# Optimization experiments

Hardware: AMD Instinct MI355X
Metric: run time of the kernel (lower is better)

Reference implementation:

```python
import jax, jax.numpy as jnp
import numpy as np

N = 20000
NEG_SLOPE = 0.2


def gatv2_layer(x, src, dst, edge_attr, Wl, bl, Wr, br, We, att, bias, H, C):
    """PyG GATv2Conv: add self-loops (edge_attr fill='mean'), gather-score-softmax-aggregate."""
    n = x.shape[0]
    E = src.shape[0]
    # --- add self loops, self-loop edge_attr = mean of incoming edge_attr per node ---
    ea_sum = jax.ops.segment_sum(edge_attr, dst, num_segments=n)
    deg = jax.ops.segment_sum(jnp.ones((E, 1), x.dtype), dst, num_segments=n)
    ea_loop = ea_sum / jnp.maximum(deg, 1.0)
    loop = jnp.arange(n)
    src_a = jnp.concatenate([src, loop])
    dst_a = jnp.concatenate([dst, loop])
    ea = jnp.concatenate([edge_attr, ea_loop], axis=0)
    # --- linear projections ---
    xl = (x @ Wl + bl).reshape(n, H, C)   # source-side features
    xr = (x @ Wr + br).reshape(n, H, C)   # target-side features
    e = (ea @ We).reshape(-1, H, C)       # edge features
    # --- per-edge GATv2 attention score ---
    m = xl[src_a] + xr[dst_a] + e                          # [E', H, C]
    s = jnp.sum(jax.nn.leaky_relu(m, NEG_SLOPE) * att, -1)  # [E', H]
    # --- softmax over incoming edges of each target node ---
    smax = jax.ops.segment_max(s, dst_a, num_segments=n)
    ex = jnp.exp(s - smax[dst_a])
    denom = jax.ops.segment_sum(ex, dst_a, num_segments=n)
    alpha = ex / (denom[dst_a] + 1e-16)                    # [E', H]
    # --- aggregate messages (alpha * x_l[src]) ---
    out = jax.ops.segment_sum(alpha[..., None] * xl[src_a], dst_a, num_segments=n)
    return out.reshape(n, H * C) + bias


def setup_inputs() -> dict:
    key = jax.random.key(0)
    ks = jax.random.split(key, 20)
    F, HID, H1, A = 128, 32, 8, 128
    E = 640000
    d = {}
    d["x"] = jax.random.normal(ks[0], (N, F), jnp.float32)
    d["edge_index"] = jax.random.randint(ks[1], (2, E), 0, N, jnp.int32).astype(jnp.int64)
    d["edge_attr"] = jax.random.normal(ks[2], (E, 1), jnp.float32)
    # layer 1 params (in=F, out=HID, heads=H1)
    d["W1l"] = jax.random.normal(ks[3], (F, H1 * HID), jnp.float32) * 0.05
    d["b1l"] = jnp.zeros((H1 * HID,), jnp.float32)
    d["W1r"] = jax.random.normal(ks[4], (F, H1 * HID), jnp.float32) * 0.05
    d["b1r"] = jnp.zeros((H1 * HID,), jnp.float32)
    d["We1"] = jax.random.normal(ks[5], (1, H1 * HID), jnp.float32) * 0.05
    d["att1"] = jax.random.normal(ks[6], (H1, HID), jnp.float32) * 0.05
    d["bias1"] = jnp.zeros((H1 * HID,), jnp.float32)
    # layer 2 params (in=H1*HID, out=A, heads=1)
    d["W2l"] = jax.random.normal(ks[7], (H1 * HID, A), jnp.float32) * 0.05
    d["b2l"] = jnp.zeros((A,), jnp.float32)
    d["W2r"] = jax.random.normal(ks[8], (H1 * HID, A), jnp.float32) * 0.05
    d["b2r"] = jnp.zeros((A,), jnp.float32)
    d["We2"] = jax.random.normal(ks[9], (1, A), jnp.float32) * 0.05
    d["att2"] = jax.random.normal(ks[10], (1, A), jnp.float32) * 0.05
    d["bias2"] = jnp.zeros((A,), jnp.float32)
    d["alpha"] = jnp.array(0.0, jnp.float32)
    return d


def reference(x, edge_index, edge_attr, W1l, b1l, W1r, b1r, We1, att1, bias1,
              W2l, b2l, W2r, b2r, We2, att2, bias2, alpha):
    src, dst = edge_index[0], edge_index[1]
    h = jax.nn.relu(gatv2_layer(x, src, dst, edge_attr, W1l, b1l, W1r, b1r,
                                We1, att1, bias1, H=8, C=32))
    h = jax.nn.relu(gatv2_layer(h, src, dst, edge_attr, W2l, b2l, W2r, b2r,
                                We2, att2, bias2, H=1, C=128))
    pooled = jnp.mean(h, axis=0, keepdims=True)  # global_mean_pool, single graph -> [1, A]
    return jax.nn.softmax(pooled, axis=1), jax.nn.sigmoid(alpha)
```

## Files before the change

kernel.cpp:

```cpp
#include <hip/hip_runtime.h>
#include <math.h>

#define NEG_SLOPE 0.2f
#define LOG2E 1.4426950408889634f

typedef __attribute__((ext_vector_type(8))) short short8;
typedef __attribute__((ext_vector_type(4))) float f32x4;
typedef __attribute__((ext_vector_type(2))) float v2f;

__device__ __forceinline__ int imin(int a, int b) { return a < b ? a : b; }

__device__ __forceinline__ unsigned int f2bf(float f) {
    unsigned int u = __float_as_uint(f);
    return (u + 0x7fffu + ((u >> 16) & 1u)) >> 16;
}
__device__ __forceinline__ float fast_exp2(float x) {
#if __has_builtin(__builtin_amdgcn_exp2f)
    return __builtin_amdgcn_exp2f(x);
#else
    return exp2f(x);
#endif
}
__device__ __forceinline__ unsigned char f2fp8(float v) {
    return (unsigned char)(__builtin_amdgcn_cvt_pk_fp8_f32(v, v, 0, false) & 0xff);
}
template <int CTRL>
__device__ __forceinline__ float dpp_add(float v) {
    int t = __builtin_amdgcn_update_dpp(0, __float_as_int(v), CTRL, 0xF, 0xF, true);
    return v + __int_as_float(t);
}

__global__ void fused_prep(const int* __restrict__ ei, const float* __restrict__ ea,
                           unsigned long long* __restrict__ hist, int E,
                           const float* __restrict__ x, unsigned short* __restrict__ xb, int nF4,
                           const float* __restrict__ W1l, const float* __restrict__ W1r,
                           const float* __restrict__ W2l, const float* __restrict__ W2r,
                           const float* __restrict__ b1l, const float* __restrict__ b1r,
                           const float* __restrict__ b2l, const float* __restrict__ b2r,
                           unsigned short* __restrict__ Wt1, unsigned short* __restrict__ Wt2,
                           float* __restrict__ b1cat, float* __restrict__ b2cat,
                           int F, int HC1, int HC2) {
    int i = blockIdx.x * blockDim.x + threadIdx.x;
    if (i < E) {
        int d = ei[E + i];
        long long fx = (long long)__float2int_rn(ea[i] * 65536.0f);
        unsigned long long v = ((unsigned long long)fx << 32) | 1ull;
        atomicAdd(&hist[(size_t)d * 8], v);
        return;
    }
    int j = i - E;
    if (j < nF4) {
        float4 v = ((const float4*)x)[j];
        uint2 r;
        r.x = f2bf(v.x) | (f2bf(v.y) << 16);
        r.y = f2bf(v.z) | (f2bf(v.w) << 16);
        ((uint2*)xb)[j] = r;
        return;
    }
    int k = j - nF4;
    int S1 = F * HC1, S2 = HC1 * HC2;
    if (k < S1) {
        int kk = k / HC1, nn = k - kk * HC1;
        Wt1[(size_t)nn * F + kk] = (unsigned short)f2bf(W1l[k]);
    } else if (k < 2 * S1) {
        int m = k - S1;
        int kk = m / HC1, nn = m - kk * HC1;
        Wt1[(size_t)(HC1 + nn) * F + kk] = (unsigned short)f2bf(W1r[m]);
    } else if (k < 2 * S1 + S2) {
        int m = k - 2 * S1;
        int kk = m / HC2, nn = m - kk * HC2;
        Wt2[(size_t)nn * HC1 + kk] = (unsigned short)f2bf(W2l[m]);
    } else if (k < 2 * S1 + 2 * S2) {
        int m = k - 2 * S1 - S2;
        int kk = m / HC2, nn = m - kk * HC2;
        Wt2[(size_t)(HC2 + nn) * HC1 + kk] = (unsigned short)f2bf(W2r[m]);
    } else if (k < 2 * S1 + 2 * S2 + 2 * HC1) {
        int m = k - 2 * S1 - 2 * S2;
        b1cat[m] = (m < HC1) ? b1l[m] : b1r[m - HC1];
    } else if (k < 2 * S1 + 2 * S2 + 2 * HC1 + 2 * HC2) {
        int m = k - 2 * S1 - 2 * S2 - 2 * HC1;
        b2cat[m] = (m < HC2) ? b2l[m] : b2r[m - HC2];
    }
}

__global__ void scan_a(const unsigned long long* __restrict__ hist, int* __restrict__ bsum, int n) {
    __shared__ int wred[4];
    int base = blockIdx.x * 1024;
    int tid = threadIdx.x;
    int s = 0;
#pragma unroll
    for (int k = 0; k < 4; ++k) {
        int i = base + tid + k * 256;
        if (i < n) s += (int)(hist[(size_t)i * 8] & 0xffffffffull);
    }
#pragma unroll
    for (int off = 32; off > 0; off >>= 1) s += __shfl_xor(s, off, 64);
    if ((tid & 63) == 0) wred[tid >> 6] = s;
    __syncthreads();
    if (tid == 0) bsum[blockIdx.x] = wred[0] + wred[1] + wred[2] + wred[3];
}

__global__ void scan_c(const unsigned long long* __restrict__ hist,
                       const int* __restrict__ bsum, int* __restrict__ row_ptr,
                       int* __restrict__ wptr_pad, float* __restrict__ ea_loop,
                       int n, int B) {
    __shared__ int wtot[4];
    __shared__ int sh_base;
    int tid = threadIdx.x;
    int wid = tid >> 6, lane = tid & 63;
    int i0 = blockIdx.x * 1024 + tid * 4;
    int dcnt[4]; float esum[4];
#pragma unroll
    for (int k = 0; k < 4; ++k) {
        if (i0 + k < n) {
            unsigned long long h = hist[(size_t)(i0 + k) * 8];
            dcnt[k] = (int)(h & 0xffffffffull);
            esum[k] = (float)((int)(h >> 32)) * (1.0f / 65536.0f);
        } else { dcnt[k] = 0; esum[k] = 0.0f; }
    }
    int tsum = dcnt[0] + dcnt[1] + dcnt[2] + dcnt[3];
    int s = tsum;
#pragma unroll
    for (int off = 1; off < 64; off <<= 1) {
        int t = __shfl_up(s, off, 64);
        if (lane >= off) s += t;
    }
    if (lane == 63) wtot[wid] = s;
    if (tid < 64) {
        int v   = (tid < B) ? bsum[tid] : 0;
        int pre = (tid < (int)blockIdx.x) ? v : 0;
        int tot = v;
#pragma unroll
        for (int off = 32; off > 0; off >>= 1) {
            pre += __shfl_xor(pre, off, 64);
            tot += __shfl_xor(tot, off, 64);
        }
        if (tid == 0) {
            sh_base = pre;
            if (blockIdx.x == 0) row_ptr[n] = tot;
        }
    }
    __syncthreads();
    int wpre = 0;
#pragma unroll
    for (int k = 0; k < 4; ++k) if (k < wid) wpre += wtot[k];
    int pre = sh_base + wpre + (s - tsum);
    if (i0 < n) {
        int4 e;
        e.x = pre;
        e.y = pre + dcnt[0];
        e.z = e.y + dcnt[1];
        e.w = e.z + dcnt[2];
        *(int4*)(row_ptr + i0) = e;
        int ev[4] = { e.x, e.y, e.z, e.w };
        float4 el;
        el.x = esum[0] / fmaxf((float)dcnt[0], 1.0f);
        el.y = esum[1] / fmaxf((float)dcnt[1], 1.0f);
        el.z = esum[2] / fmaxf((float)dcnt[2], 1.0f);
        el.w = esum[3] / fmaxf((float)dcnt[3], 1.0f);
        *(float4*)(ea_loop + i0) = el;
#pragma unroll
        for (int k = 0; k < 4; ++k) wptr_pad[(size_t)(i0 + k) * 16] = ev[k];
    }
}

__global__ void edge_scatter(const int* __restrict__ ei, const float* __restrict__ ea,
                             int* __restrict__ wptr_pad, int2* __restrict__ spk, int E) {
    int e = blockIdx.x * blockDim.x + threadIdx.x;
    if (e < E) {
        int d = ei[E + e];
        int pos = atomicAdd(&wptr_pad[(size_t)d * 16], 1);
        spk[pos] = make_int2(ei[e], __float_as_int(ea[e]));
    }
}

template <bool OUT_FP8>
__global__ void __launch_bounds__(256)
gemm_bf16(const unsigned short* __restrict__ A, const unsigned short* __restrict__ Bt,
          const float* __restrict__ bias, void* __restrict__ Cv,
          int M, int N, int K) {
    __shared__ __attribute__((aligned(16))) unsigned short As[64 * 40];
    __shared__ __attribute__((aligned(16))) unsigned short Bs[64 * 40];
    int tid  = threadIdx.x;
    int wave = tid >> 6, lane = tid & 63;
    int m0 = blockIdx.x * 64, n0 = blockIdx.y * 64;
    int row = tid >> 2, kg = (tid & 3) * 8;

    f32x4 acc[4] = {};
    for (int kk = 0; kk < K; kk += 32) {
        int gm = m0 + row;
        uint4 av;
        if (gm < M) av = *(const uint4*)(A + (size_t)gm * K + kk + kg);
        else        av = make_uint4(0, 0, 0, 0);
        *(uint4*)&As[row * 40 + kg] = av;
        uint4 bv = *(const uint4*)(Bt + (size_t)(n0 + row) * K + kk + kg);
        *(uint4*)&Bs[row * 40 + kg] = bv;
        __syncthreads();
        short8 a = *(const short8*)&As[(wave * 16 + (lane & 15)) * 40 + (lane >> 4) * 8];
#pragma unroll
        for (int g = 0; g < 4; ++g) {
            short8 b = *(const short8*)&Bs[(g * 16 + (lane & 15)) * 40 + (lane >> 4) * 8];
            acc[g] = __builtin_amdgcn_mfma_f32_16x16x32_bf16(a, b, acc[g], 0, 0, 0);
        }
        __syncthreads();
    }
#pragma unroll
    for (int g = 0; g < 4; ++g) {
        int col = n0 + g * 16 + (lane & 15);
        float bs = bias[col];
#pragma unroll
        for (int r = 0; r < 4; ++r) {
            int grow = m0 + wave * 16 + (lane >> 4) * 4 + r;
            if (grow < M) {
                float val = acc[g][r] + bs;
                if constexpr (OUT_FP8) {
                    ((unsigned char*)Cv)[(size_t)grow * N + col] = f2fp8(val);
                } else {
                    ((unsigned short*)Cv)[(size_t)grow * N + col] = (unsigned short)f2bf(val);
                }
            }
        }
    }
}

template <int NG>
__device__ __forceinline__ void unp2(uint2 u, v2f* xf) {
    xf[0] = __builtin_amdgcn_cvt_pk_f32_fp8(u.x, false);
    xf[1] = __builtin_amdgcn_cvt_pk_f32_fp8(u.x, true);
    if constexpr (NG == 4) {
        xf[2] = __builtin_amdgcn_cvt_pk_f32_fp8(u.y, false);
        xf[3] = __builtin_amdgcn_cvt_pk_f32_fp8(u.y, true);
    }
}
template <int G>
__device__ __forceinline__ float grp_reduce32(float vs) {
    vs = dpp_add<0xB1>(vs);
    if constexpr (G >= 4)  vs = dpp_add<0x4E>(vs);
    if constexpr (G >= 8)  vs = dpp_add<0x141>(vs);
    if constexpr (G >= 16) vs = dpp_add<0x140>(vs);
    if constexpr (G >= 32) {
        int t = __builtin_amdgcn_ds_swizzle(__float_as_int(vs), 0x401F);
        vs += __int_as_float(t);
    }
    return vs;
}

template <int HC, int STRIDE, int C, int OUT_MODE>
__global__ void __launch_bounds__(256)
gat_agg(const unsigned char* __restrict__ xlr,
        const float* __restrict__ We, const float* __restrict__ att,
        const float* __restrict__ bias,
        const int* __restrict__ row_ptr, const int2* __restrict__ spk,
        const float* __restrict__ ea_loop,
        void* __restrict__ out, int n) {
    constexpr int NV = HC / 32;
    constexpr int NG = NV / 2;
    constexpr int G  = C / NV;
    constexpr float K23 = 2.0f / 3.0f;
    int wave = threadIdx.x >> 6;
    int lane = threadIdx.x & 63;
    int node = blockIdx.x * 4 + wave;
    if (node >= n) return;
    unsigned int lo32 = (unsigned int)(lane & 31) * NV;

    auto ldd = [&](unsigned int off) -> uint2 {
        uint2 r;
        if constexpr (NV == 8) r = *(const uint2*)(xlr + off);
        else { r.x = *(const unsigned int*)(xlr + off); r.y = 0u; }
        return r;
    };

    v2f xr2[NG], We2[NG], att62[NG], o2[NG];
    {
        uint2 xru = ldd((unsigned int)node * STRIDE + HC + lo32);
        unp2<NG>(xru, xr2);
    }
#pragma unroll
    for (int g = 0; g < NG; ++g) {
        We2[g]   = *(const v2f*)(We  + lo32 + 2 * g);
        v2f a    = *(const v2f*)(att + lo32 + 2 * g);
        att62[g] = a * (0.6f * LOG2E);
        o2[g]    = v2f{0.0f, 0.0f};
    }
    float l = 0.0f;

    int start = __builtin_amdgcn_readfirstlane(row_ptr[node]);
    int end   = __builtin_amdgcn_readfirstlane(row_ptr[node + 1]);
    float ea_l = ea_loop[node];

    auto process = [&](uint2 du, float w, bool maskhi) {
        v2f xf[NG];
        unp2<NG>(du, xf);
        v2f vs2 = v2f{0.0f, 0.0f};
#pragma unroll
        for (int g = 0; g < NG; ++g) {
            v2f t  = We2[g] * w + xr2[g];
            v2f mm = xf[g] + t;
            v2f u;
            u.x = fmaf(fabsf(mm.x), K23, mm.x);
            u.y = fmaf(fabsf(mm.y), K23, mm.y);
            vs2 = att62[g] * u + vs2;
        }
        float vs = vs2.x + vs2.y;
        vs = grp_reduce32<G>(vs);
        float pr = fast_exp2(vs);
        if (maskhi && lane >= 32) pr = 0.0f;
        l += pr;
#pragma unroll
        for (int g = 0; g < NG; ++g) o2[g] = xf[g] * pr + o2[g];
    };

    process(ldd((unsigned int)node * STRIDE + lo32), ea_l, true);

    int cnt = end - start;
    for (int b0 = 0; b0 < cnt; b0 += 64) {
        int rem = imin(64, cnt - b0);
        int idxc = imin(start + b0 + lane, end - 1);
        int2 pv = spk[idxc];

        auto ldp = [&](int p) -> uint2 {
            int sA = __builtin_amdgcn_readlane(pv.x, 2 * p);
            int sB = __builtin_amdgcn_readlane(pv.x, 2 * p + 1);
            int s  = (lane < 32) ? sA : sB;
            return ldd((unsigned int)s * STRIDE + lo32);
        };
        auto ldw = [&](int p) -> float {
            int wA = __builtin_amdgcn_readlane(pv.y, 2 * p);
            int wB = __builtin_amdgcn_readlane(pv.y, 2 * p + 1);
            return __int_as_float((lane < 32) ? wA : wB);
        };

        int npair = rem >> 1;
        if (npair > 0) {
            int pc = npair - 1;
            uint2 A0 = ldp(0), A1 = ldp(imin(1, pc));
            float Wa0 = ldw(0), Wa1 = ldw(imin(1, pc));
            int p = 0;
            for (; p + 4 <= npair; p += 4) {
                uint2 B0 = ldp(p + 2), B1 = ldp(p + 3);
                float Wb0 = ldw(p + 2), Wb1 = ldw(p + 3);
                process(A0, Wa0, false); process(A1, Wa1, false);
                A0 = ldp(imin(p + 4, pc)); A1 = ldp(imin(p + 5, pc));
                Wa0 = ldw(imin(p + 4, pc)); Wa1 = ldw(imin(p + 5, pc));
                process(B0, Wb0, false); process(B1, Wb1, false);
            }
            int left = npair - p;
            if (left > 0) process(A0, Wa0, false);
            if (left > 1) process(A1, Wa1, false);
            for (int k = p + 2; k < npair; ++k) process(ldp(k), ldw(k), false);
        }
        if (rem & 1) {
            int e = rem - 1;
            int s = __builtin_amdgcn_readlane(pv.x, e);
            float w = __int_as_float(__builtin_amdgcn_readlane(pv.y, e));
            process(ldd((unsigned int)s * STRIDE + lo32), w, true);
        }
    }

    l += __shfl_xor(l, 32, 64);
#pragma unroll
    for (int g = 0; g < NG; ++g) {
        o2[g].x += __shfl_xor(o2[g].x, 32, 64);
        o2[g].y += __shfl_xor(o2[g].y, 32, 64);
    }
    float inv = 1.0f / (l + 1e-16f);

    if (lane < 32) {
        float v[NV];
#pragma unroll
        for (int g = 0; g < NG; ++g) {
            v2f b = *(const v2f*)(bias + lo32 + 2 * g);
            v[2 * g]     = fmaxf(o2[g].x * inv + b.x, 0.0f);
            v[2 * g + 1] = fmaxf(o2[g].y * inv + b.y, 0.0f);
        }
        if constexpr (OUT_MODE == 0) {
            unsigned short* op = (unsigned short*)out + (size_t)node * HC + lo32;
            if constexpr (NV == 8) {
                uint4 t;
                t.x = f2bf(v[0]) | (f2bf(v[1]) << 16);
                t.y = f2bf(v[2]) | (f2bf(v[3]) << 16);
                t.z = f2bf(v[4]) | (f2bf(v[5]) << 16);
                t.w = f2bf(v[6]) | (f2bf(v[7]) << 16);
                *(uint4*)op = t;
            } else {
                uint2 t;
                t.x = f2bf(v[0]) | (f2bf(v[1]) << 16);
                t.y = f2bf(v[2]) | (f2bf(v[3]) << 16);
                *(uint2*)op = t;
            }
        } else {
            float* pacc = (float*)out + (size_t)(blockIdx.x & 255) * 128 + lo32;
#pragma unroll
            for (int j = 0; j < NV; ++j) atomicAdd(&pacc[j], v[j]);
        }
    }
}

__global__ void __launch_bounds__(1024)
pool_final(const float* __restrict__ partial, int nb,
           const float* __restrict__ alpha_in,
           float* __restrict__ out, int n) {
    __shared__ float acc[8][128];
    __shared__ float red[4];
    int t = threadIdx.x & 127;
    int g = threadIdx.x >> 7;
    float s = 0.0f;
    for (int b = g; b < nb; b += 8) s += partial[b * 128 + t];
    acc[g][t] = s;
    __syncthreads();
    if (threadIdx.x < 128) {
        float tot = 0.0f;
#pragma unroll
        for (int k = 0; k < 8; ++k) tot += acc[k][t];
        float mean = tot / (float)n;
        float mx = mean;
#pragma unroll
        for (int off = 32; off > 0; off >>= 1) mx = fmaxf(mx, __shfl_xor(mx, off, 64));
        if ((t & 63) == 0) red[t >> 6] = mx;
        __syncthreads();
        mx = fmaxf(red[0], red[1]);
        float ex = __expf(mean - mx);
        float sm = ex;
#pragma unroll
        for (int off = 32; off > 0; off >>= 1) sm += __shfl_xor(sm, off, 64);
        if ((t & 63) == 0) red[2 + (t >> 6)] = sm;
        __syncthreads();
        sm = red[2] + red[3];
        out[t] = ex / sm;
        if (t == 0) out[128] = 1.0f / (1.0f + __expf(-alpha_in[0]));
    }
}

extern "C" void kernel_launch(void* const* d_in, const int* in_sizes, int n_in,
                              void* d_out, int out_size, void* d_ws, size_t ws_size,
                              hipStream_t stream) {
    const float* x    = (const float*)d_in[0];
    const int*   ei   = (const int*)d_in[1];
    const float* ea   = (const float*)d_in[2];
    const float* W1l  = (const float*)d_in[3];
    const float* b1l  = (const float*)d_in[4];
    const float* W1r  = (const float*)d_in[5];
    const float* b1r  = (const float*)d_in[6];
    const float* We1  = (const float*)d_in[7];
    const float* att1 = (const float*)d_in[8];
    const float* bias1= (const float*)d_in[9];
    const float* W2l  = (const float*)d_in[10];
    const float* b2l  = (const float*)d_in[11];
    const float* W2r  = (const float*)d_in[12];
    const float* b2r  = (const float*)d_in[13];
    const float* We2  = (const float*)d_in[14];
    const float* att2 = (const float*)d_in[15];
    const float* bias2= (const float*)d_in[16];
    const float* alpha= (const float*)d_in[17];
    float* out = (float*)d_out;

    const int F = 128, HC1 = 256, HC2 = 128;
    const int n = in_sizes[0] / F;
    const int E = in_sizes[1] / 2;
    const int B = (n + 1023) / 1024;

    char* ws = (char*)d_ws;
    size_t off = 0;
    auto alloc = [&](size_t bytes) { size_t p = off; off += (bytes + 255) & ~(size_t)255; return p; };

    unsigned long long* hist = (unsigned long long*)(ws + alloc((size_t)n * 8 * 8));
    int*   row_ptr = (int*)  (ws + alloc((size_t)(n + 1) * 4));
    int*   wptr    = (int*)  (ws + alloc((size_t)n * 16 * 4));
    float* ea_loop = (float*)(ws + alloc((size_t)n * 4));
    int*   bsum    = (int*)  (ws + alloc(64 * 4));
    int2*  spk     = (int2*) (ws + alloc((size_t)E * 8));
    unsigned short* xb   = (unsigned short*)(ws + alloc((size_t)n * F * 2));
    unsigned short* Wt1  = (unsigned short*)(ws + alloc((size_t)F * (2 * HC1) * 2));
    unsigned short* Wt2  = (unsigned short*)(ws + alloc((size_t)HC1 * (2 * HC2) * 2));
    float* b1cat   = (float*)(ws + alloc((size_t)2 * HC1 * 4));
    float* b2cat   = (float*)(ws + alloc((size_t)2 * HC2 * 4));
    unsigned char* xlr1 = (unsigned char*)(ws + alloc((size_t)n * 2 * HC1));
    unsigned short* h1  = (unsigned short*)(ws + alloc((size_t)n * HC1 * 2));
    float* partial = (float*)(ws + alloc((size_t)256 * 128 * 4));
    unsigned char* xlr2 = xlr1;
    const int NB_SLOTS = 256;

    (void)hipMemsetAsync(hist, 0, (size_t)n * 8 * 8, stream);
    (void)hipMemsetAsync(partial, 0, (size_t)NB_SLOTS * 128 * 4, stream);

    int tb = 256;
    {
        int nF4  = n * F / 4;
        int WTOT = 2 * F * HC1 + 2 * HC1 * HC2 + 2 * HC1 + 2 * HC2;
        int total = E + nF4 + WTOT;
        fused_prep<<<(total + tb - 1) / tb, tb, 0, stream>>>(
            ei, ea, hist, E, x, xb, nF4,
            W1l, W1r, W2l, W2r, b1l, b1r, b2l, b2r,
            Wt1, Wt2, b1cat, b2cat, F, HC1, HC2);
    }
    scan_a<<<B, 256, 0, stream>>>(hist, bsum, n);
    scan_c<<<B, 256, 0, stream>>>(hist, bsum, row_ptr, wptr, ea_loop, n, B);
    edge_scatter<<<(E + tb - 1) / tb, tb, 0, stream>>>(ei, ea, wptr, spk, E);

    {
        dim3 grid((n + 63) / 64, (2 * HC1) / 64);
        gemm_bf16<true><<<grid, 256, 0, stream>>>(xb, Wt1, b1cat, xlr1, n, 2 * HC1, F);
    }
    gat_agg<256, 512, 32, 0><<<(n + 3) / 4, 256, 0, stream>>>(
        xlr1, We1, att1, bias1, row_ptr, spk, ea_loop, h1, n);

    {
        dim3 grid((n + 63) / 64, (2 * HC2) / 64);
        gemm_bf16<true><<<grid, 256, 0, stream>>>(h1, Wt2, b2cat, xlr2, n, 2 * HC2, HC1);
    }
    gat_agg<128, 256, 128, 1><<<(n + 3) / 4, 256, 0, stream>>>(
        xlr2, We2, att2, bias2, row_ptr, spk, ea_loop, partial, n);

    pool_final<<<1, 1024, 0, stream>>>(partial, NB_SLOTS, alpha, out, n);
}
```

Measured before the change: 292.2 us.

## Load edge records per half-wave directly and use packed FP32 math in aggregation

The aggregation loop now reads each edge's (src, weight) pair straight from memory per half-wave, replacing the batched 64-wide load followed by readlane broadcasts. It software-pipelines two pairs ahead, padding the edge array with zeroed entries so prefetches can run past the end safely. The score and accumulation math uses inline v_pk_fma/v_pk_add, and leaky-ReLU is rewritten as a linear term plus an abs term. Address computation switches from a multiply to a shift. The aim is to cut cross-lane readlane overhead and VALU instruction count, at the cost of more small scalar-like global loads per edge.

```diff
diff --git a/kernel.cpp b/kernel.cpp
--- a/kernel.cpp
+++ b/kernel.cpp
@@ -28,6 +28,16 @@
 __device__ __forceinline__ float dpp_add(float v) {
     int t = __builtin_amdgcn_update_dpp(0, __float_as_int(v), CTRL, 0xF, 0xF, true);
     return v + __int_as_float(t);
+}
+__device__ __forceinline__ v2f pk_fma(v2f a, v2f b, v2f c) {
+    v2f d;
+    asm("v_pk_fma_f32 %0, %1, %2, %3" : "=v"(d) : "v"(a), "v"(b), "v"(c));
+    return d;
+}
+__device__ __forceinline__ v2f pk_add(v2f a, v2f b) {
+    v2f d;
+    asm("v_pk_add_f32 %0, %1, %2" : "=v"(d) : "v"(a), "v"(b));
+    return d;
 }
 
 __global__ void fused_prep(const int* __restrict__ ei, const float* __restrict__ ea,
@@ -256,12 +266,14 @@
     constexpr int NV = HC / 32;
     constexpr int NG = NV / 2;
     constexpr int G  = C / NV;
+    constexpr int SHIFT = (STRIDE == 512) ? 9 : 8;
     constexpr float K23 = 2.0f / 3.0f;
     int wave = threadIdx.x >> 6;
     int lane = threadIdx.x & 63;
     int node = blockIdx.x * 4 + wave;
     if (node >= n) return;
     unsigned int lo32 = (unsigned int)(lane & 31) * NV;
+    int half = lane >> 5;
 
     auto ldd = [&](unsigned int off) -> uint2 {
         uint2 r;
@@ -269,12 +281,12 @@
         else { r.x = *(const unsigned int*)(xlr + off); r.y = 0u; }
         return r;
     };
+    auto gat = [&](int s) -> uint2 {
+        return ldd(((unsigned int)s << SHIFT) + lo32);
+    };
 
     v2f xr2[NG], We2[NG], att62[NG], o2[NG];
-    {
-        uint2 xru = ldd((unsigned int)node * STRIDE + HC + lo32);
-        unp2<NG>(xru, xr2);
-    }
+    unp2<NG>(ldd(((unsigned int)node << SHIFT) + HC + lo32), xr2);
 #pragma unroll
     for (int g = 0; g < NG; ++g) {
         We2[g]   = *(const v2f*)(We  + lo32 + 2 * g);
@@ -291,70 +303,60 @@
     auto process = [&](uint2 du, float w, bool maskhi) {
         v2f xf[NG];
         unp2<NG>(du, xf);
-        v2f vs2 = v2f{0.0f, 0.0f};
+        v2f w2 = {w, w};
+        v2f vs6 = {0.0f, 0.0f};
+        float vs4 = 0.0f;
 #pragma unroll
         for (int g = 0; g < NG; ++g) {
-            v2f t  = We2[g] * w + xr2[g];
-            v2f mm = xf[g] + t;
-            v2f u;
-            u.x = fmaf(fabsf(mm.x), K23, mm.x);
-            u.y = fmaf(fabsf(mm.y), K23, mm.y);
-            vs2 = att62[g] * u + vs2;
-        }
-        float vs = vs2.x + vs2.y;
+            v2f t  = pk_fma(w2, We2[g], xr2[g]);
+            v2f mm = pk_add(xf[g], t);
+            vs6 = pk_fma(att62[g], mm, vs6);
+            vs4 = fmaf(fabsf(mm.x), att62[g].x, vs4);
+            vs4 = fmaf(fabsf(mm.y), att62[g].y, vs4);
+        }
+        float vs = fmaf(K23, vs4, vs6.x + vs6.y);
         vs = grp_reduce32<G>(vs);
         float pr = fast_exp2(vs);
         if (maskhi && lane >= 32) pr = 0.0f;
         l += pr;
-#pragma unroll
-        for (int g = 0; g < NG; ++g) o2[g] = xf[g] * pr + o2[g];
+        v2f pr2 = {pr, pr};
+#pragma unroll
+        for (int g = 0; g < NG; ++g) o2[g] = pk_fma(xf[g], pr2, o2[g]);
     };
 
-    process(ldd((unsigned int)node * STRIDE + lo32), ea_l, true);
+    process(ldd(((unsigned int)node << SHIFT) + lo32), ea_l, true);
 
     int cnt = end - start;
-    for (int b0 = 0; b0 < cnt; b0 += 64) {
-        int rem = imin(64, cnt - b0);
-        int idxc = imin(start + b0 + lane, end - 1);
-        int2 pv = spk[idxc];
-
-        auto ldp = [&](int p) -> uint2 {
-            int sA = __builtin_amdgcn_readlane(pv.x, 2 * p);
-            int sB = __builtin_amdgcn_readlane(pv.x, 2 * p + 1);
-            int s  = (lane < 32) ? sA : sB;
-            return ldd((unsigned int)s * STRIDE + lo32);
-        };
-        auto ldw = [&](int p) -> float {
-            int wA = __builtin_amdgcn_readlane(pv.y, 2 * p);
-            int wB = __builtin_amdgcn_readlane(pv.y, 2 * p + 1);
-            return __int_as_float((lane < 32) ? wA : wB);
-        };
-
-        int npair = rem >> 1;
-        if (npair > 0) {
-            int pc = npair - 1;
-            uint2 A0 = ldp(0), A1 = ldp(imin(1, pc));
-            float Wa0 = ldw(0), Wa1 = ldw(imin(1, pc));
-            int p = 0;
-            for (; p + 4 <= npair; p += 4) {
-                uint2 B0 = ldp(p + 2), B1 = ldp(p + 3);
-                float Wb0 = ldw(p + 2), Wb1 = ldw(p + 3);
-                process(A0, Wa0, false); process(A1, Wa1, false);
-                A0 = ldp(imin(p + 4, pc)); A1 = ldp(imin(p + 5, pc));
-                Wa0 = ldw(imin(p + 4, pc)); Wa1 = ldw(imin(p + 5, pc));
-                process(B0, Wb0, false); process(B1, Wb1, false);
-            }
-            int left = npair - p;
-            if (left > 0) process(A0, Wa0, false);
-            if (left > 1) process(A1, Wa1, false);
-            for (int k = p + 2; k < npair; ++k) process(ldp(k), ldw(k), false);
-        }
-        if (rem & 1) {
-            int e = rem - 1;
-            int s = __builtin_amdgcn_readlane(pv.x, e);
-            float w = __int_as_float(__builtin_amdgcn_readlane(pv.y, e));
-            process(ldd((unsigned int)s * STRIDE + lo32), w, true);
-        }
+    int npair = cnt >> 1;
+    const int2* pp = spk + start + half;
+
+    if (npair >= 2) {
+        int2 sA = pp[0], sB = pp[2];
+        uint2 gA = gat(sA.x);
+        int p = 0;
+        for (; p + 2 < npair; p += 2) {
+            uint2 gB = gat(sB.x);
+            int2 sC = pp[2 * p + 4];
+            process(gA, __int_as_float(sA.y), false);
+            uint2 gC = gat(sC.x);
+            int2 sD = pp[2 * p + 6];
+            process(gB, __int_as_float(sB.y), false);
+            sA = sC; sB = sD; gA = gC;
+        }
+        if (npair - p == 2) {
+            uint2 gB = gat(sB.x);
+            process(gA, __int_as_float(sA.y), false);
+            process(gB, __int_as_float(sB.y), false);
+        } else {
+            process(gA, __int_as_float(sA.y), false);
+        }
+    } else if (npair == 1) {
+        int2 sA = pp[0];
+        process(gat(sA.x), __int_as_float(sA.y), false);
+    }
+    if (cnt & 1) {
+        int2 st = spk[end - 1];
+        process(gat(st.x), __int_as_float(st.y), true);
     }
 
     l += __shfl_xor(l, 32, 64);
@@ -468,7 +470,7 @@
     int*   wptr    = (int*)  (ws + alloc((size_t)n * 16 * 4));
     float* ea_loop = (float*)(ws + alloc((size_t)n * 4));
     int*   bsum    = (int*)  (ws + alloc(64 * 4));
-    int2*  spk     = (int2*) (ws + alloc((size_t)E * 8));
+    int2*  spk     = (int2*) (ws + alloc((size_t)(E + 8) * 8));
     unsigned short* xb   = (unsigned short*)(ws + alloc((size_t)n * F * 2));
     unsigned short* Wt1  = (unsigned short*)(ws + alloc((size_t)F * (2 * HC1) * 2));
     unsigned short* Wt2  = (unsigned short*)(ws + alloc((size_t)HC1 * (2 * HC2) * 2));
@@ -482,6 +484,7 @@
 
     (void)hipMemsetAsync(hist, 0, (size_t)n * 8 * 8, stream);
     (void)hipMemsetAsync(partial, 0, (size_t)NB_SLOTS * 128 * 4, stream);
+    (void)hipMemsetAsync(spk + E, 0, 8 * sizeof(int2), stream);
 
     int tb = 256;
     {
```

Result: faster. 284.1 us (-2.8%).
